# Kernel tuning notes

Measured on AMD Instinct MI355X. Metric: run time of the kernel, lower is better.

Reference implementation:

```python
import jax, jax.numpy as jnp
import numpy as np

B = 4096; CPG = 2; NPC = 25              # graphs, components/graph, nodes/component
N = B * CPG * NPC; C = B * CPG; E = 409600
IN_CH = 128; HID = 256; L = 3; S = 64; M = 8; NCLS = 2
BN_EPS = 1e-5

def _leaky(x):
    return jax.nn.leaky_relu(x, 0.01)

def _gin_conv(x, src, dst, wa, ba, wb, bb):
    # GINConv with eps=0: mlp(x + sum_{j in N(i)} x_j); messages flow src->dst
    agg = jnp.zeros_like(x).at[dst].add(x[src])
    h = x + agg
    return jax.nn.relu(h @ wa + ba) @ wb + bb

def setup_inputs():
    key = jax.random.key(0)
    ks = jax.random.split(key, 12)
    rn = lambda k, shp: jax.random.normal(k, shp, jnp.float32) * 0.05
    return {
        "x": jax.random.normal(ks[0], (N, IN_CH), jnp.float32),
        "w0a": rn(ks[1], (IN_CH, HID)), "b0a": jnp.zeros((HID,), jnp.float32),
        "w0b": rn(ks[2], (HID, HID)), "b0b": jnp.zeros((HID,), jnp.float32),
        "wra": rn(ks[3], (L - 1, HID, HID)), "bra": jnp.zeros((L - 1, HID), jnp.float32),
        "wrb": rn(ks[4], (L - 1, HID, HID)), "brb": jnp.zeros((L - 1, HID), jnp.float32),
        "Wc": jax.random.uniform(ks[5], (HID, S * M), jnp.float32, -1.0, 1.0),
        "fc1_w": rn(ks[6], (S, 32)), "fc1_b": jnp.zeros((32,), jnp.float32),
        "bn_g": jnp.ones((32,), jnp.float32), "bn_b": jnp.zeros((32,), jnp.float32),
        "fc2_w": rn(ks[7], (32, NCLS)), "fc2_b": jnp.zeros((NCLS,), jnp.float32),
        "edge_index": jax.random.randint(ks[8], (2, E), 0, N, jnp.int32),
        "node2comp": (jnp.arange(N, dtype=jnp.int32) // NPC),
        "comp2graph": (jnp.arange(C, dtype=jnp.int32) // CPG),
        "comp_pos": (jnp.arange(C, dtype=jnp.int32) % CPG),
        "n_graphs": B,
        "max_comps": CPG,
    }

def reference(x, w0a, b0a, w0b, b0b, wra, bra, wrb, brb, Wc, fc1_w, fc1_b, bn_g, bn_b, fc2_w, fc2_b, edge_index, node2comp, comp2graph, comp_pos, n_graphs, max_comps):
    src, dst = edge_index[0], edge_index[1]
    # --- GIN backbone (num_layers convs, ReLU between layers) ---
    h = _gin_conv(x, src, dst, w0a, b0a, w0b, b0b)
    for i in range(wra.shape[0]):
        h = jax.nn.relu(h)
        h = _gin_conv(h, src, dst, wra[i], bra[i], wrb[i], brb[i])
    # --- per-connected-component mean pooling ---
    n_comp = comp2graph.shape[0]
    comp_sum = jax.ops.segment_sum(h, node2comp, num_segments=n_comp)           # [C, d]
    comp_size = jax.ops.segment_sum(jnp.ones((h.shape[0],), h.dtype), node2comp, num_segments=n_comp)
    # torch.mean over the zero-padded cardinality dim divides by the per-graph MAX component size
    graph_maxc = jax.ops.segment_max(comp_size, comp2graph, num_segments=n_graphs)
    comp_mean = comp_sum / graph_maxc[comp2graph][:, None]
    # --- pad components into [B, max_comps, d] ---
    X = jnp.zeros((n_graphs, max_comps, h.shape[1]), h.dtype).at[comp2graph, comp_pos].set(comp_mean)
    # --- set-rep classifier ---
    t = _leaky(jnp.einsum('bcd,dk->bck', X, Wc))                                # [B, maxC, S*M]
    s = fc1_w.shape[0]; m = Wc.shape[1] // s
    t = t.reshape(t.shape[0], t.shape[1], m, s)                                 # view(B, maxC, n_elements, n_hidden_sets)
    t = jnp.max(t, axis=2)
    t = jnp.sum(t, axis=1)                                                      # [B, S]
    t = t @ fc1_w + fc1_b
    mu = jnp.mean(t, axis=0); var = jnp.var(t, axis=0)                          # BN, batch stats (track_running_stats=False)
    t = (t - mu) / jnp.sqrt(var + BN_EPS) * bn_g + bn_b
    t = _leaky(t)
    out = t @ fc2_w + fc2_b
    return jax.nn.log_softmax(out, axis=1)
```

## Files before the change

### kernel.cpp

```cpp
#include <hip/hip_runtime.h>
#include <hip/hip_fp16.h>
#include <math.h>

typedef unsigned short u16;
typedef float f32x4 __attribute__((ext_vector_type(4)));
typedef __bf16 bf16x8 __attribute__((ext_vector_type(8)));

__device__ __forceinline__ float b2f(u16 u) {
    union { unsigned int i; float f; } v; v.i = ((unsigned int)u) << 16; return v.f;
}
__device__ __forceinline__ u16 f2b(float f) {
    union { float f; unsigned int i; } v; v.f = f;
    unsigned int lsb = (v.i >> 16) & 1u;
    return (u16)((v.i + 0x7fffu + lsb) >> 16);
}

__device__ __forceinline__ void gld16(const u16* g, u16* l) {
    __builtin_amdgcn_global_load_lds(
        (const __attribute__((address_space(1))) unsigned int*)g,
        (__attribute__((address_space(3))) unsigned int*)l,
        16, 0, 0);
}

__global__ __launch_bounds__(256)
void k_count(const int* __restrict__ dst, int* __restrict__ cnt, int E)
{
    int e = blockIdx.x * 256 + threadIdx.x;
    if (e < E) atomicAdd(&cnt[dst[e]], 1);
}

__global__ __launch_bounds__(256)
void k_scan1(const int* __restrict__ cnt, int* __restrict__ rowptr,
             int* __restrict__ bsum, int N)
{
    __shared__ int s[256];
    int t = threadIdx.x, i = blockIdx.x * 256 + t;
    int v = (i < N) ? cnt[i] : 0;
    s[t] = v;
    __syncthreads();
#pragma unroll
    for (int off = 1; off < 256; off <<= 1) {
        int add = (t >= off) ? s[t - off] : 0;
        __syncthreads();
        s[t] += add;
        __syncthreads();
    }
    if (i < N) rowptr[i] = s[t] - v;
    if (t == 255) bsum[blockIdx.x] = s[255];
}

__global__ __launch_bounds__(256)
void k_scan2(const int* __restrict__ bsum, int* __restrict__ bscan, int nb)
{
    __shared__ int s[256];
    int t = threadIdx.x;
    int g[4], e[4];
    int base = t * 4;
#pragma unroll
    for (int j = 0; j < 4; ++j) g[j] = (base + j < nb) ? bsum[base + j] : 0;
    e[0] = 0; e[1] = g[0]; e[2] = g[0] + g[1]; e[3] = g[0] + g[1] + g[2];
    int tsum = e[3] + g[3];
    s[t] = tsum;
    __syncthreads();
#pragma unroll
    for (int off = 1; off < 256; off <<= 1) {
        int add = (t >= off) ? s[t - off] : 0;
        __syncthreads();
        s[t] += add;
        __syncthreads();
    }
    int texcl = s[t] - tsum;
#pragma unroll
    for (int j = 0; j < 4; ++j)
        if (base + j < nb) bscan[base + j] = texcl + e[j];
}

__global__ __launch_bounds__(256)
void k_scan3(int* __restrict__ rowptr, const int* __restrict__ bscan,
             int* __restrict__ cursor, int N)
{
    int i = blockIdx.x * 256 + threadIdx.x;
    if (i >= N) return;
    int r = rowptr[i] + bscan[i >> 8];
    rowptr[i] = r;
    cursor[i] = r;
}

__global__ __launch_bounds__(256)
void k_fill(const int* __restrict__ src, const int* __restrict__ dst,
            int* __restrict__ cursor, int* __restrict__ col, int E)
{
    int e = blockIdx.x * 256 + threadIdx.x;
    if (e >= E) return;
    int pos = atomicAdd(&cursor[dst[e]], 1);
    col[pos] = src[e];
}

template<int F, bool RELU, bool F32SRC>
__global__ __launch_bounds__(256)
void k_aggr(const void* __restrict__ hsrc, const int* __restrict__ cnt,
            const int* __restrict__ rowptr, const int* __restrict__ col,
            u16* __restrict__ aeff, int N)
{
    constexpr int CPE = F / 8;
    int tid = blockIdx.x * 256 + threadIdx.x;
    int node = tid / CPE, c = tid % CPE;
    if (node >= N) return;
    int n = cnt[node], rp = rowptr[node];
    float acc[8];
    if (F32SRC) {
        const float* p = (const float*)hsrc + (size_t)node * F + c * 8;
        float4 a = *(const float4*)p, b = *(const float4*)(p + 4);
        float xv[8] = {a.x, a.y, a.z, a.w, b.x, b.y, b.z, b.w};
#pragma unroll
        for (int i = 0; i < 8; ++i) acc[i] = RELU ? fmaxf(xv[i], 0.f) : xv[i];
    } else {
        u16 vs[8] __attribute__((aligned(16)));
        *(uint4*)vs = *(const uint4*)((const u16*)hsrc + (size_t)node * F + c * 8);
#pragma unroll
        for (int i = 0; i < 8; ++i) {
            float x = b2f(vs[i]);
            acc[i] = RELU ? fmaxf(x, 0.f) : x;
        }
    }
    for (int j = 0; j < n; ++j) {
        int s = col[rp + j];
        if (F32SRC) {
            const float* p = (const float*)hsrc + (size_t)s * F + c * 8;
            float4 a = *(const float4*)p, b = *(const float4*)(p + 4);
            float xv[8] = {a.x, a.y, a.z, a.w, b.x, b.y, b.z, b.w};
#pragma unroll
            for (int i = 0; i < 8; ++i) acc[i] += RELU ? fmaxf(xv[i], 0.f) : xv[i];
        } else {
            u16 vs[8] __attribute__((aligned(16)));
            *(uint4*)vs = *(const uint4*)((const u16*)hsrc + (size_t)s * F + c * 8);
#pragma unroll
            for (int i = 0; i < 8; ++i) {
                float x = b2f(vs[i]);
                acc[i] += RELU ? fmaxf(x, 0.f) : x;
            }
        }
    }
    u16 ob[8] __attribute__((aligned(16)));
#pragma unroll
    for (int i = 0; i < 8; ++i) ob[i] = f2b(acc[i]);
    *(uint4*)(aeff + (size_t)node * F + c * 8) = *(const uint4*)ob;
}

__global__ void k_T(const float* __restrict__ in, u16* __restrict__ out, int K, int N)
{
    int t = blockIdx.x * 256 + threadIdx.x;
    if (t >= K * N) return;
    int n = t / K, k = t % K;
    out[t] = f2b(in[k * N + n]);
}

template<int K>
__global__ __launch_bounds__(256)
void k_gin(const u16* __restrict__ Aeff,
           const u16* __restrict__ WaT, const float* __restrict__ ba,
           const u16* __restrict__ WbT, const float* __restrict__ bb,
           u16* __restrict__ Hout)
{
    __shared__ u16 As2[64 * 32];
    __shared__ u16 Bs2[256 * 32];
    __shared__ u16 Hs2[64 * 256];

    const int tid = threadIdx.x, lane = tid & 63, wave = tid >> 6;
    const int bm0 = blockIdx.x * 64;
    const int lc = lane & 15, lr = (lane >> 4) * 4;
    const int cw0 = wave * 64;
    const int l15 = lane & 15, lq = lane >> 4;

    u16* aDst = As2 + wave * 512;
    const u16* aRow = Aeff + (size_t)(bm0 + wave * 16 + l15) * K + lq * 8;

    f32x4 acc[4][4];
#pragma unroll
    for (int r = 0; r < 4; ++r)
#pragma unroll
        for (int c = 0; c < 4; ++c) acc[r][c] = (f32x4){0.f, 0.f, 0.f, 0.f};

    for (int k0 = 0; k0 < K; k0 += 32) {
        gld16(aRow + k0, aDst);
#pragma unroll
        for (int c = 0; c < 4; ++c)
            gld16(WaT + (size_t)(cw0 + c * 16 + l15) * K + k0 + lq * 8,
                  Bs2 + (wave * 4 + c) * 512);
        __syncthreads();
        bf16x8 a[4], b[4];
#pragma unroll
        for (int r = 0; r < 4; ++r) a[r] = *(const bf16x8*)&As2[(r * 64 + lane) * 8];
#pragma unroll
        for (int c = 0; c < 4; ++c) b[c] = *(const bf16x8*)&Bs2[((wave * 4 + c) * 64 + lane) * 8];
#pragma unroll
        for (int r = 0; r < 4; ++r)
#pragma unroll
            for (int c = 0; c < 4; ++c)
                acc[r][c] = __builtin_amdgcn_mfma_f32_16x16x32_bf16(a[r], b[c], acc[r][c], 0, 0, 0);
        __syncthreads();
    }

#pragma unroll
    for (int c = 0; c < 4; ++c) {
        const int n = cw0 + c * 16 + lc;
        const float bv = ba[n];
        const int nb = (n >> 5) * 256 + ((n >> 3) & 3) * 16;
#pragma unroll
        for (int r = 0; r < 4; ++r)
#pragma unroll
            for (int i = 0; i < 4; ++i)
                Hs2[(nb + r * 64 + lr + i) * 8 + (n & 7)] = f2b(fmaxf(acc[r][c][i] + bv, 0.f));
    }
    __syncthreads();

    f32x4 acc2[4][4];
#pragma unroll
    for (int r = 0; r < 4; ++r)
#pragma unroll
        for (int c = 0; c < 4; ++c) acc2[r][c] = (f32x4){0.f, 0.f, 0.f, 0.f};
    for (int k0 = 0; k0 < 256; k0 += 32) {
#pragma unroll
        for (int c = 0; c < 4; ++c)
            gld16(WbT + (size_t)(cw0 + c * 16 + l15) * 256 + k0 + lq * 8,
                  Bs2 + (wave * 4 + c) * 512);
        __syncthreads();
        bf16x8 a[4], b[4];
#pragma unroll
        for (int r = 0; r < 4; ++r)
            a[r] = *(const bf16x8*)&Hs2[((k0 >> 5) * 256 + r * 64 + lane) * 8];
#pragma unroll
        for (int c = 0; c < 4; ++c) b[c] = *(const bf16x8*)&Bs2[((wave * 4 + c) * 64 + lane) * 8];
#pragma unroll
        for (int r = 0; r < 4; ++r)
#pragma unroll
            for (int c = 0; c < 4; ++c)
                acc2[r][c] = __builtin_amdgcn_mfma_f32_16x16x32_bf16(a[r], b[c], acc2[r][c], 0, 0, 0);
        __syncthreads();
    }
#pragma unroll
    for (int c = 0; c < 4; ++c) {
        const int n = cw0 + c * 16 + lc;
        const float bv = bb[n];
#pragma unroll
        for (int r = 0; r < 4; ++r)
#pragma unroll
            for (int i = 0; i < 4; ++i)
                Hout[(size_t)(bm0 + r * 16 + lr + i) * 256 + n] = f2b(acc2[r][c][i] + bv);
    }
}

__global__ __launch_bounds__(256)
void k_lin(const u16* __restrict__ A, const u16* __restrict__ WT,
           float* __restrict__ C)
{
    __shared__ u16 As[64 * 40];
    __shared__ u16 Bs[256 * 40];
    const int tid = threadIdx.x, lane = tid & 63, wave = tid >> 6;
    const int bm0 = blockIdx.x * 64, bn0 = blockIdx.y * 256;
    const int fm = lane & 15, fk = (lane >> 4) * 8;
    const int lc = lane & 15, lr = (lane >> 4) * 4;
    const int cw0 = wave * 64;
    const int sr = tid >> 2, sc = tid & 3;

    f32x4 acc[4][4];
#pragma unroll
    for (int r = 0; r < 4; ++r)
#pragma unroll
        for (int c = 0; c < 4; ++c) acc[r][c] = (f32x4){0.f, 0.f, 0.f, 0.f};

    for (int k0 = 0; k0 < 256; k0 += 32) {
        *(uint4*)&As[sr * 40 + sc * 8] =
            *(const uint4*)(A + (size_t)(bm0 + sr) * 256 + k0 + sc * 8);
        {
            const uint4* wp = (const uint4*)(WT + (size_t)(bn0 + tid) * 256 + k0);
#pragma unroll
            for (int c = 0; c < 4; ++c)
                *(uint4*)&Bs[tid * 40 + c * 8] = wp[c];
        }
        __syncthreads();
        bf16x8 a[4], b[4];
#pragma unroll
        for (int r = 0; r < 4; ++r) a[r] = *(const bf16x8*)&As[(r * 16 + fm) * 40 + fk];
#pragma unroll
        for (int c = 0; c < 4; ++c) b[c] = *(const bf16x8*)&Bs[(cw0 + c * 16 + fm) * 40 + fk];
#pragma unroll
        for (int r = 0; r < 4; ++r)
#pragma unroll
            for (int c = 0; c < 4; ++c)
                acc[r][c] = __builtin_amdgcn_mfma_f32_16x16x32_bf16(a[r], b[c], acc[r][c], 0, 0, 0);
        __syncthreads();
    }
#pragma unroll
    for (int c = 0; c < 4; ++c) {
        const int col = bn0 + cw0 + c * 16 + lc;
#pragma unroll
        for (int r = 0; r < 4; ++r)
#pragma unroll
            for (int i = 0; i < 4; ++i) {
                float v = acc[r][c][i];
                v = (v >= 0.f) ? v : 0.01f * v;
                C[(size_t)(bm0 + r * 16 + lr + i) * 512 + col] = v;
            }
    }
}

__global__ void k_pool(const u16* __restrict__ H, u16* __restrict__ Xc)
{
    int c = blockIdx.x, f = threadIdx.x;
    const u16* p = H + (size_t)c * 25 * 256 + f;
    float s = 0.f;
#pragma unroll
    for (int j = 0; j < 25; ++j) s += b2f(p[j * 256]);
    Xc[(size_t)c * 256 + f] = f2b(s / 25.0f);
}

__global__ void k_setpool(const float* __restrict__ T, float* __restrict__ Tp)
{
    int tid = blockIdx.x * 256 + threadIdx.x;
    int b = tid >> 6, s = tid & 63;
    float acc = 0.f;
#pragma unroll
    for (int c = 0; c < 2; ++c) {
        const float* row = T + ((size_t)(b * 2 + c)) * 512 + s;
        float mx = row[0];
#pragma unroll
        for (int m = 1; m < 8; ++m) mx = fmaxf(mx, row[m * 64]);
        acc += mx;
    }
    Tp[tid] = acc;
}

__global__ void k_fc1(const float* __restrict__ Tp, const float* __restrict__ w,
                      const float* __restrict__ b, float* __restrict__ T1)
{
    int tid = blockIdx.x * 256 + threadIdx.x;
    int bb = tid >> 5, j = tid & 31;
    float s = b[j];
#pragma unroll
    for (int k = 0; k < 64; ++k) s += Tp[bb * 64 + k] * w[k * 32 + j];
    T1[tid] = s;
}

__global__ void k_bnstats(const float* __restrict__ T1, float* __restrict__ stats)
{
    __shared__ float r1[256], r2[256];
    const int j = blockIdx.x, t = threadIdx.x;
    float s = 0.f, ss = 0.f;
    for (int b = t; b < 4096; b += 256) {
        float v = T1[b * 32 + j];
        s += v; ss += v * v;
    }
    r1[t] = s; r2[t] = ss;
    __syncthreads();
    for (int off = 128; off > 0; off >>= 1) {
        if (t < off) { r1[t] += r1[t + off]; r2[t] += r2[t + off]; }
        __syncthreads();
    }
    if (t == 0) {
        float mu  = r1[0] * (1.f / 4096.f);
        float var = r2[0] * (1.f / 4096.f) - mu * mu;
        stats[j]      = mu;
        stats[32 + j] = 1.f / sqrtf(var + 1e-5f);
    }
}

__global__ void k_head(const float* __restrict__ T1, const float* __restrict__ stats,
                       const float* __restrict__ g, const float* __restrict__ bb,
                       const float* __restrict__ w2, const float* __restrict__ b2,
                       float* __restrict__ out)
{
    const int b = blockIdx.x * 256 + threadIdx.x;
    float l0 = b2[0], l1 = b2[1];
#pragma unroll
    for (int j = 0; j < 32; ++j) {
        float v = (T1[b * 32 + j] - stats[j]) * stats[32 + j] * g[j] + bb[j];
        v = (v >= 0.f) ? v : 0.01f * v;
        l0 += v * w2[j * 2];
        l1 += v * w2[j * 2 + 1];
    }
    float mx  = fmaxf(l0, l1);
    float lse = mx + logf(expf(l0 - mx) + expf(l1 - mx));
    out[b * 2]     = l0 - lse;
    out[b * 2 + 1] = l1 - lse;
}

extern "C" void kernel_launch(void* const* d_in, const int* in_sizes, int n_in,
                              void* d_out, int out_size, void* d_ws, size_t ws_size,
                              hipStream_t stream)
{
    (void)n_in; (void)out_size; (void)ws_size;
    constexpr int NN = 204800, NCOMP = 8192, NGRAPH = 4096;

    const float* x    = (const float*)d_in[0];
    const float* w0a  = (const float*)d_in[1];
    const float* b0a  = (const float*)d_in[2];
    const float* w0b  = (const float*)d_in[3];
    const float* b0b  = (const float*)d_in[4];
    const float* wra  = (const float*)d_in[5];
    const float* bra  = (const float*)d_in[6];
    const float* wrb  = (const float*)d_in[7];
    const float* brb  = (const float*)d_in[8];
    const float* Wc   = (const float*)d_in[9];
    const float* f1w  = (const float*)d_in[10];
    const float* f1b  = (const float*)d_in[11];
    const float* bng  = (const float*)d_in[12];
    const float* bnb  = (const float*)d_in[13];
    const float* f2w  = (const float*)d_in[14];
    const float* f2bb = (const float*)d_in[15];
    const int* ei   = (const int*)d_in[16];
    const int  E    = in_sizes[16] / 2;
    const int* src  = ei;
    const int* dst  = ei + E;

    char* ws = (char*)d_ws;
    u16*    AEFF = (u16*)ws;
    u16*    H   = (u16*)(ws + (size_t)104857600);
    u16*    wt  = (u16*)(ws + (size_t)209715200);
    u16 *WT0 = wt, *WT1 = wt + 65536, *WT2 = wt + 131072, *WT3 = wt + 196608,
        *WT4 = wt + 262144, *WT5 = wt + 327680, *WT6 = wt + 393216;
    char* csr = ws + (size_t)210763776;
    int* cnt    = (int*)csr;
    int* rowptr = (int*)(csr + 819200);
    int* cursor = (int*)(csr + 1638400);
    int* col    = (int*)(csr + 2457600);
    int* bsum   = (int*)(csr + 4096000);
    int* bscan  = (int*)(csr + 4100096);
    u16*   Xc    = (u16*)ws;
    float* Tfull = (float*)(ws + (size_t)16777216);
    float* Tp    = (float*)(ws + (size_t)33554432);
    float* T1    = (float*)(ws + (size_t)41943040);
    float* stats = (float*)(ws + (size_t)46137344);

    const dim3 blk(256);
    const int NB = NN / 256;

    hipMemsetAsync(cnt, 0, NN * 4, stream);
    k_count<<<(E + 255) / 256, blk, 0, stream>>>(dst, cnt, E);
    k_scan1<<<NB, blk, 0, stream>>>(cnt, rowptr, bsum, NN);
    k_scan2<<<1, blk, 0, stream>>>(bsum, bscan, NB);
    k_scan3<<<NB, blk, 0, stream>>>(rowptr, bscan, cursor, NN);
    k_fill<<<(E + 255) / 256, blk, 0, stream>>>(src, dst, cursor, col, E);

    k_T<<<128, blk, 0, stream>>>(w0a, WT0, 128, 256);
    k_T<<<256, blk, 0, stream>>>(w0b, WT1, 256, 256);
    k_T<<<256, blk, 0, stream>>>(wra,          WT2, 256, 256);
    k_T<<<256, blk, 0, stream>>>(wra + 65536,  WT3, 256, 256);
    k_T<<<256, blk, 0, stream>>>(wrb,          WT4, 256, 256);
    k_T<<<256, blk, 0, stream>>>(wrb + 65536,  WT5, 256, 256);
    k_T<<<512, blk, 0, stream>>>(Wc, WT6, 256, 512);

    k_aggr<128, false, true><<<(NN * 16) / 256, blk, 0, stream>>>(x, cnt, rowptr, col, AEFF, NN);
    k_gin<128><<<NN / 64, blk, 0, stream>>>(AEFF, WT0, b0a, WT1, b0b, H);

    const u16* WA[2] = {WT2, WT3};
    const u16* WB[2] = {WT4, WT5};
    for (int l = 0; l < 2; ++l) {
        k_aggr<256, true, false><<<(NN * 32) / 256, blk, 0, stream>>>(H, cnt, rowptr, col, AEFF, NN);
        k_gin<256><<<NN / 64, blk, 0, stream>>>(
            AEFF, WA[l], bra + (size_t)l * 256, WB[l], brb + (size_t)l * 256, H);
    }

    k_pool<<<NCOMP, blk, 0, stream>>>(H, Xc);
    k_lin<<<dim3(NCOMP / 64, 2), blk, 0, stream>>>(Xc, WT6, Tfull);
    k_setpool<<<(NGRAPH * 64) / 256, blk, 0, stream>>>(Tfull, Tp);
    k_fc1<<<(NGRAPH * 32) / 256, blk, 0, stream>>>(Tp, f1w, f1b, T1);
    k_bnstats<<<32, blk, 0, stream>>>(T1, stats);
    k_head<<<NGRAPH / 256, blk, 0, stream>>>(T1, stats, bng, bnb, f2w, f2bb, (float*)d_out);
}
```

Before: 806.5 us.

## Fuse neighbor aggregation into GIN MLP kernel via shared-memory gather

Removes the separate aggregation kernel and performs the CSR neighbor sum inside the GIN kernel, writing the bf16 result directly into shared memory as the first GEMM's A operand. This eliminates the intermediate aggregated-feature buffer's global write and reread and one launch per layer, and ping-pongs the hidden buffers between layers. The gather now uses 4 threads per node, each accumulating 32 features in registers. That reduces gather parallelism and coalescing and raises register pressure. The first weight tile load is also hoisted ahead of the gather.

Measured after the change: 890.6 us. 1.1x slower.

```diff
diff --git a/kernel.cpp b/kernel.cpp
--- a/kernel.cpp
+++ b/kernel.cpp
@@ -96,57 +96,6 @@
     col[pos] = src[e];
 }
 
-template<int F, bool RELU, bool F32SRC>
-__global__ __launch_bounds__(256)
-void k_aggr(const void* __restrict__ hsrc, const int* __restrict__ cnt,
-            const int* __restrict__ rowptr, const int* __restrict__ col,
-            u16* __restrict__ aeff, int N)
-{
-    constexpr int CPE = F / 8;
-    int tid = blockIdx.x * 256 + threadIdx.x;
-    int node = tid / CPE, c = tid % CPE;
-    if (node >= N) return;
-    int n = cnt[node], rp = rowptr[node];
-    float acc[8];
-    if (F32SRC) {
-        const float* p = (const float*)hsrc + (size_t)node * F + c * 8;
-        float4 a = *(const float4*)p, b = *(const float4*)(p + 4);
-        float xv[8] = {a.x, a.y, a.z, a.w, b.x, b.y, b.z, b.w};
-#pragma unroll
-        for (int i = 0; i < 8; ++i) acc[i] = RELU ? fmaxf(xv[i], 0.f) : xv[i];
-    } else {
-        u16 vs[8] __attribute__((aligned(16)));
-        *(uint4*)vs = *(const uint4*)((const u16*)hsrc + (size_t)node * F + c * 8);
-#pragma unroll
-        for (int i = 0; i < 8; ++i) {
-            float x = b2f(vs[i]);
-            acc[i] = RELU ? fmaxf(x, 0.f) : x;
-        }
-    }
-    for (int j = 0; j < n; ++j) {
-        int s = col[rp + j];
-        if (F32SRC) {
-            const float* p = (const float*)hsrc + (size_t)s * F + c * 8;
-            float4 a = *(const float4*)p, b = *(const float4*)(p + 4);
-            float xv[8] = {a.x, a.y, a.z, a.w, b.x, b.y, b.z, b.w};
-#pragma unroll
-            for (int i = 0; i < 8; ++i) acc[i] += RELU ? fmaxf(xv[i], 0.f) : xv[i];
-        } else {
-            u16 vs[8] __attribute__((aligned(16)));
-            *(uint4*)vs = *(const uint4*)((const u16*)hsrc + (size_t)s * F + c * 8);
-#pragma unroll
-            for (int i = 0; i < 8; ++i) {
-                float x = b2f(vs[i]);
-                acc[i] += RELU ? fmaxf(x, 0.f) : x;
-            }
-        }
-    }
-    u16 ob[8] __attribute__((aligned(16)));
-#pragma unroll
-    for (int i = 0; i < 8; ++i) ob[i] = f2b(acc[i]);
-    *(uint4*)(aeff + (size_t)node * F + c * 8) = *(const uint4*)ob;
-}
-
 __global__ void k_T(const float* __restrict__ in, u16* __restrict__ out, int K, int N)
 {
     int t = blockIdx.x * 256 + threadIdx.x;
@@ -155,16 +104,17 @@
     out[t] = f2b(in[k * N + n]);
 }
 
-template<int K>
-__global__ __launch_bounds__(256)
-void k_gin(const u16* __restrict__ Aeff,
+template<int K, bool RELU, bool F32SRC>
+__global__ __launch_bounds__(256)
+void k_gin(const void* __restrict__ hsrc,
+           const int* __restrict__ cnt, const int* __restrict__ rowptr,
+           const int* __restrict__ col,
            const u16* __restrict__ WaT, const float* __restrict__ ba,
            const u16* __restrict__ WbT, const float* __restrict__ bb,
            u16* __restrict__ Hout)
 {
-    __shared__ u16 As2[64 * 32];
+    __shared__ u16 AH[64 * 256];
     __shared__ u16 Bs2[256 * 32];
-    __shared__ u16 Hs2[64 * 256];
 
     const int tid = threadIdx.x, lane = tid & 63, wave = tid >> 6;
     const int bm0 = blockIdx.x * 64;
@@ -172,34 +122,99 @@
     const int cw0 = wave * 64;
     const int l15 = lane & 15, lq = lane >> 4;
 
-    u16* aDst = As2 + wave * 512;
-    const u16* aRow = Aeff + (size_t)(bm0 + wave * 16 + l15) * K + lq * 8;
-
-    f32x4 acc[4][4];
+#pragma unroll
+    for (int c = 0; c < 4; ++c)
+        gld16(WaT + (size_t)(cw0 + c * 16 + l15) * K + lq * 8,
+              Bs2 + (wave * 4 + c) * 512);
+
+    {
+        const int r    = tid >> 2;
+        const int seg  = tid & 3;
+        const int node = bm0 + r;
+        const int nn = cnt[node], rp = rowptr[node];
+        constexpr int KSEG = K / 4;
+        constexpr int NP   = KSEG / 32;
+        u16* const wbase = AH + (r >> 4) * 512 + (r & 15) * 8;
+#pragma unroll
+        for (int p = 0; p < NP; ++p) {
+            const int k0 = seg * KSEG + p * 32;
+            float acc[32];
+#pragma unroll
+            for (int i = 0; i < 32; ++i) acc[i] = 0.f;
+            for (int j = -1; j < nn; ++j) {
+                const int sIdx = (j < 0) ? node : col[rp + j];
+                if (F32SRC) {
+                    const float4* q = (const float4*)((const float*)hsrc + (size_t)sIdx * K + k0);
+#pragma unroll
+                    for (int cc = 0; cc < 8; ++cc) {
+                        float4 v = q[cc];
+                        if (RELU) {
+                            v.x = fmaxf(v.x, 0.f); v.y = fmaxf(v.y, 0.f);
+                            v.z = fmaxf(v.z, 0.f); v.w = fmaxf(v.w, 0.f);
+                        }
+                        acc[cc * 4 + 0] += v.x; acc[cc * 4 + 1] += v.y;
+                        acc[cc * 4 + 2] += v.z; acc[cc * 4 + 3] += v.w;
+                    }
+                } else {
+                    const uint4* q = (const uint4*)((const u16*)hsrc + (size_t)sIdx * K + k0);
+#pragma unroll
+                    for (int cc = 0; cc < 4; ++cc) {
+                        u16 vs[8] __attribute__((aligned(16)));
+                        *(uint4*)vs = q[cc];
+#pragma unroll
+                        for (int i2 = 0; i2 < 8; ++i2) {
+                            float x = b2f(vs[i2]);
+                            acc[cc * 8 + i2] += RELU ? fmaxf(x, 0.f) : x;
+                        }
+                    }
+                }
+            }
+            u16* wp = wbase + (k0 >> 5) * 2048;
+#pragma unroll
+            for (int kc = 0; kc < 4; ++kc) {
+                u16 tmp[8] __attribute__((aligned(16)));
+#pragma unroll
+                for (int jj = 0; jj < 8; ++jj) tmp[jj] = f2b(acc[kc * 8 + jj]);
+                *(uint4*)(wp + kc * 128) = *(const uint4*)tmp;
+            }
+        }
+    }
+    __syncthreads();
+
+    constexpr int NK1 = K / 32;
+    f32x4 acc1[4][4];
 #pragma unroll
     for (int r = 0; r < 4; ++r)
 #pragma unroll
-        for (int c = 0; c < 4; ++c) acc[r][c] = (f32x4){0.f, 0.f, 0.f, 0.f};
-
-    for (int k0 = 0; k0 < K; k0 += 32) {
-        gld16(aRow + k0, aDst);
+        for (int c = 0; c < 4; ++c) acc1[r][c] = (f32x4){0.f, 0.f, 0.f, 0.f};
+
+    for (int kb = 0; kb < NK1; ++kb) {
+        bf16x8 a[4], b[4];
+#pragma unroll
+        for (int r = 0; r < 4; ++r)
+            a[r] = *(const bf16x8*)&AH[(kb * 256 + r * 64 + lane) * 8];
 #pragma unroll
         for (int c = 0; c < 4; ++c)
-            gld16(WaT + (size_t)(cw0 + c * 16 + l15) * K + k0 + lq * 8,
-                  Bs2 + (wave * 4 + c) * 512);
-        __syncthreads();
-        bf16x8 a[4], b[4];
-#pragma unroll
-        for (int r = 0; r < 4; ++r) a[r] = *(const bf16x8*)&As2[(r * 64 + lane) * 8];
-#pragma unroll
-        for (int c = 0; c < 4; ++c) b[c] = *(const bf16x8*)&Bs2[((wave * 4 + c) * 64 + lane) * 8];
-#pragma unroll
-        for (int r = 0; r < 4; ++r)
-#pragma unroll
-            for (int c = 0; c < 4; ++c)
-                acc[r][c] = __builtin_amdgcn_mfma_f32_16x16x32_bf16(a[r], b[c], acc[r][c], 0, 0, 0);
-        __syncthreads();
-    }
+            b[c] = *(const bf16x8*)&Bs2[((wave * 4 + c) * 64 + lane) * 8];
+#pragma unroll
+        for (int r = 0; r < 4; ++r)
+#pragma unroll
+            for (int c = 0; c < 4; ++c)
+                acc1[r][c] = __builtin_amdgcn_mfma_f32_16x16x32_bf16(a[r], b[c], acc1[r][c], 0, 0, 0);
+        __syncthreads();
+        if (kb + 1 < NK1) {
+#pragma unroll
+            for (int c = 0; c < 4; ++c)
+                gld16(WaT + (size_t)(cw0 + c * 16 + l15) * K + (kb + 1) * 32 + lq * 8,
+                      Bs2 + (wave * 4 + c) * 512);
+            __syncthreads();
+        }
+    }
+
+#pragma unroll
+    for (int c = 0; c < 4; ++c)
+        gld16(WbT + (size_t)(cw0 + c * 16 + l15) * 256 + lq * 8,
+              Bs2 + (wave * 4 + c) * 512);
 
 #pragma unroll
     for (int c = 0; c < 4; ++c) {
@@ -210,7 +225,7 @@
         for (int r = 0; r < 4; ++r)
 #pragma unroll
             for (int i = 0; i < 4; ++i)
-                Hs2[(nb + r * 64 + lr + i) * 8 + (n & 7)] = f2b(fmaxf(acc[r][c][i] + bv, 0.f));
+                AH[(nb + r * 64 + lr + i) * 8 + (n & 7)] = f2b(fmaxf(acc1[r][c][i] + bv, 0.f));
     }
     __syncthreads();
 
@@ -219,24 +234,28 @@
     for (int r = 0; r < 4; ++r)
 #pragma unroll
         for (int c = 0; c < 4; ++c) acc2[r][c] = (f32x4){0.f, 0.f, 0.f, 0.f};
-    for (int k0 = 0; k0 < 256; k0 += 32) {
+
+    for (int kb = 0; kb < 8; ++kb) {
+        bf16x8 a[4], b[4];
+#pragma unroll
+        for (int r = 0; r < 4; ++r)
+            a[r] = *(const bf16x8*)&AH[(kb * 256 + r * 64 + lane) * 8];
 #pragma unroll
         for (int c = 0; c < 4; ++c)
-            gld16(WbT + (size_t)(cw0 + c * 16 + l15) * 256 + k0 + lq * 8,
-                  Bs2 + (wave * 4 + c) * 512);
-        __syncthreads();
-        bf16x8 a[4], b[4];
-#pragma unroll
-        for (int r = 0; r < 4; ++r)
-            a[r] = *(const bf16x8*)&Hs2[((k0 >> 5) * 256 + r * 64 + lane) * 8];
-#pragma unroll
-        for (int c = 0; c < 4; ++c) b[c] = *(const bf16x8*)&Bs2[((wave * 4 + c) * 64 + lane) * 8];
+            b[c] = *(const bf16x8*)&Bs2[((wave * 4 + c) * 64 + lane) * 8];
 #pragma unroll
         for (int r = 0; r < 4; ++r)
 #pragma unroll
             for (int c = 0; c < 4; ++c)
                 acc2[r][c] = __builtin_amdgcn_mfma_f32_16x16x32_bf16(a[r], b[c], acc2[r][c], 0, 0, 0);
         __syncthreads();
+        if (kb < 7) {
+#pragma unroll
+            for (int c = 0; c < 4; ++c)
+                gld16(WbT + (size_t)(cw0 + c * 16 + l15) * 256 + (kb + 1) * 32 + lq * 8,
+                      Bs2 + (wave * 4 + c) * 512);
+            __syncthreads();
+        }
     }
 #pragma unroll
     for (int c = 0; c < 4; ++c) {
@@ -414,8 +433,8 @@
     const int* dst  = ei + E;
 
     char* ws = (char*)d_ws;
-    u16*    AEFF = (u16*)ws;
-    u16*    H   = (u16*)(ws + (size_t)104857600);
+    u16*    H1  = (u16*)ws;
+    u16*    H0  = (u16*)(ws + (size_t)104857600);
     u16*    wt  = (u16*)(ws + (size_t)209715200);
     u16 *WT0 = wt, *WT1 = wt + 65536, *WT2 = wt + 131072, *WT3 = wt + 196608,
         *WT4 = wt + 262144, *WT5 = wt + 327680, *WT6 = wt + 393216;
@@ -450,18 +469,14 @@
     k_T<<<256, blk, 0, stream>>>(wrb + 65536,  WT5, 256, 256);
     k_T<<<512, blk, 0, stream>>>(Wc, WT6, 256, 512);
 
-    k_aggr<128, false, true><<<(NN * 16) / 256, blk, 0, stream>>>(x, cnt, rowptr, col, AEFF, NN);
-    k_gin<128><<<NN / 64, blk, 0, stream>>>(AEFF, WT0, b0a, WT1, b0b, H);
-
-    const u16* WA[2] = {WT2, WT3};
-    const u16* WB[2] = {WT4, WT5};
-    for (int l = 0; l < 2; ++l) {
-        k_aggr<256, true, false><<<(NN * 32) / 256, blk, 0, stream>>>(H, cnt, rowptr, col, AEFF, NN);
-        k_gin<256><<<NN / 64, blk, 0, stream>>>(
-            AEFF, WA[l], bra + (size_t)l * 256, WB[l], brb + (size_t)l * 256, H);
-    }
-
-    k_pool<<<NCOMP, blk, 0, stream>>>(H, Xc);
+    k_gin<128, false, true><<<NN / 64, blk, 0, stream>>>(
+        x, cnt, rowptr, col, WT0, b0a, WT1, b0b, H0);
+    k_gin<256, true, false><<<NN / 64, blk, 0, stream>>>(
+        H0, cnt, rowptr, col, WT2, bra, WT4, brb, H1);
+    k_gin<256, true, false><<<NN / 64, blk, 0, stream>>>(
+        H1, cnt, rowptr, col, WT3, bra + 256, WT5, brb + 256, H0);
+
+    k_pool<<<NCOMP, blk, 0, stream>>>(H0, Xc);
     k_lin<<<dim3(NCOMP / 64, 2), blk, 0, stream>>>(Xc, WT6, Tfull);
     k_setpool<<<(NGRAPH * 64) / 256, blk, 0, stream>>>(Tfull, Tp);
     k_fc1<<<(NGRAPH * 32) / 256, blk, 0, stream>>>(Tp, f1w, f1b, T1);
```
